# Performance work log

Measured on AMD Instinct MI355X. Metric: run time of the kernel, lower is better.

## Reference

```python
import jax, jax.numpy as jnp
import numpy as np
from jax import lax

BETA = 0.25


def setup_inputs() -> dict:
    key = jax.random.key(0)
    k1, k2 = jax.random.split(key)
    z = jax.random.normal(k1, (16, 64, 32, 32), dtype=jnp.float32)
    # codebook initialized uniform(-1/K, 1/K) in the original; small random is fine for a baseline
    weight = jax.random.uniform(k2, (8192, 64), dtype=jnp.float32, minval=-1.0 / 8192, maxval=1.0 / 8192)
    return {"z": z, "weight": weight}


def reference(z, weight):
    B, D, H, W = z.shape  # D == embedding_dim
    zf = jnp.transpose(z, (0, 2, 3, 1)).reshape(-1, D)  # [N, D]
    # squared L2 distances: ||z||^2 - 2 z.W^T + ||W||^2  -> [N, K]
    dist = (jnp.sum(zf * zf, axis=1, keepdims=True)
            - 2.0 * jnp.matmul(zf, weight.T)
            + jnp.sum(weight * weight, axis=1))
    idx = jnp.argmin(dist, axis=1)  # [N]
    qe = weight[idx]  # [N, D] gather
    quantized = jnp.transpose(qe.reshape(B, H, W, D), (0, 3, 1, 2))  # back to NCHW
    codebook_loss = jnp.mean((qe - lax.stop_gradient(zf)) ** 2)
    commitment_loss = BETA * jnp.mean((zf - lax.stop_gradient(qe)) ** 2)
    # straight-through estimator
    quantized_st = z + lax.stop_gradient(quantized - z)
    return quantized_st, commitment_loss, codebook_loss
```

## Files before the change

### kernel.cpp

```cpp
#include <hip/hip_runtime.h>
#include <hip/hip_bf16.h>
#include <stdint.h>


typedef __bf16 bf16x8 __attribute__((ext_vector_type(8)));
typedef float f32x16 __attribute__((ext_vector_type(16)));

__global__ __launch_bounds__(256)
void vq_prep(const float* __restrict__ w, __bf16* __restrict__ wbf,
             float* __restrict__ wnneg, float* __restrict__ out)
{
  const int i = blockIdx.x * 256 + threadIdx.x;
  const float v = w[i];
  wbf[i] = (__bf16)v;
  float s = v * v;
#pragma unroll
  for (int m = 1; m < 64; m <<= 1) s += __shfl_xor(s, m);
  if ((threadIdx.x & 63) == 0) wnneg[i >> 6] = -0.5f * s;
  if (blockIdx.x == 0 && threadIdx.x < 2) out[1048576 + threadIdx.x] = 0.0f;
}

__global__ __launch_bounds__(512, 2)
void vq_argmax(const float* __restrict__ z, const __bf16* __restrict__ wbf,
               const float* __restrict__ wnneg, float* __restrict__ cand)
{
  __shared__ __align__(16) char bufs[3][16384];
  __shared__ __align__(16) float wnl[1024];
  const int t = threadIdx.x;
  const int lane = t & 63, wv = t >> 6;
  const int hi = lane >> 5, hi4 = hi << 2, rA = lane & 31;
  const int ksp = blockIdx.x & 7, zgrp = blockIdx.x >> 3;
  const int kbase = ksp << 10;
  const int b = zgrp >> 2;
  const int hw0 = (zgrp & 3) << 8;
  const int ch = wv >> 1, rg = wv & 1;

  ((float2*)wnl)[t] = ((const float2*)(wnneg + kbase))[t];
  asm volatile("s_waitcnt lgkmcnt(0)" ::: "memory");

  auto STAGE = [&](int s) {
    char* buf = &bufs[s % 3][0];
    if (s < 4) {
      const char* src = (const char*)z
          + (((size_t)((b << 6) + (s << 4) + wv)) << 12) + (hw0 << 2) + (lane << 4);
      __builtin_amdgcn_global_load_lds(
          (const __attribute__((address_space(1))) void*)src,
          (__attribute__((address_space(3))) void*)(buf + (wv << 10)), 16, 0, 0);
      __builtin_amdgcn_global_load_lds(
          (const __attribute__((address_space(1))) void*)(src + ((size_t)8 << 12)),
          (__attribute__((address_space(3))) void*)(buf + 8192 + (wv << 10)), 16, 0, 0);
    } else {
      const int st = s - 4;
      const int tt = t & 255;
      const int row = tt >> 3, slot = (tt & 7) ^ (row & 7);
      const int q0 = t >> 8, q1 = q0 + 2;
      const char* wb = (const char*)wbf;
      const char* s0 = wb + (((size_t)(kbase + (q0 << 8) + (st << 5) + row)) << 7) + (slot << 4);
      const char* s1 = wb + (((size_t)(kbase + (q1 << 8) + (st << 5) + row)) << 7) + (slot << 4);
      char* d0 = buf + (q0 << 12) + ((wv & 3) << 10);
      char* d1 = buf + (q1 << 12) + ((wv & 3) << 10);
      __builtin_amdgcn_global_load_lds((const __attribute__((address_space(1))) void*)s0,
          (__attribute__((address_space(3))) void*)d0, 16, 0, 0);
      __builtin_amdgcn_global_load_lds((const __attribute__((address_space(1))) void*)s1,
          (__attribute__((address_space(3))) void*)d1, 16, 0, 0);
    }
  };

  STAGE(0); STAGE(1);

  bf16x8 zf[4][4];
#pragma unroll
  for (int c = 0; c < 4; ++c) {
    asm volatile("s_waitcnt vmcnt(2)" ::: "memory");
    asm volatile("s_barrier" ::: "memory");
    const float* zp = (const float*)(&bufs[c % 3][0] + (hi << 13));
#pragma unroll
    for (int nt = 0; nt < 4; ++nt) {
      const int nl = (rg << 7) + (nt << 5) + rA;
      bf16x8 zv;
#pragma unroll
      for (int j = 0; j < 8; ++j) zv[j] = (__bf16)zp[(j << 8) + nl];
      zf[nt][c] = zv;
    }
    STAGE(c + 2);
  }

  float bestpk[4] = {-3.0e38f, -3.0e38f, -3.0e38f, -3.0e38f};

#pragma unroll 1
  for (int i = 4; i < 12; ++i) {
    if (i < 11) asm volatile("s_waitcnt vmcnt(2)" ::: "memory");
    else        asm volatile("s_waitcnt vmcnt(0)" ::: "memory");
    asm volatile("s_barrier" ::: "memory");
    const int st = i - 4;
    const char* tb = &bufs[i % 3][0] + (ch << 12);

    bf16x8 af[4];
#pragma unroll
    for (int ks = 0; ks < 4; ++ks) {
      const int c16 = (ks << 1) + hi;
      af[ks] = *(const bf16x8*)(tb + (rA << 7) + ((c16 ^ (rA & 7)) << 4));
    }

    const int kloc = (ch << 8) + (st << 5);
    f32x16 acc[4];
#pragma unroll
    for (int nt = 0; nt < 4; ++nt) {
      const float4 q0 = *(const float4*)(wnl + kloc + hi4);
      const float4 q1 = *(const float4*)(wnl + kloc + 8 + hi4);
      const float4 q2 = *(const float4*)(wnl + kloc + 16 + hi4);
      const float4 q3 = *(const float4*)(wnl + kloc + 24 + hi4);
      acc[nt] = (f32x16){q0.x, q0.y, q0.z, q0.w, q1.x, q1.y, q1.z, q1.w,
                         q2.x, q2.y, q2.z, q2.w, q3.x, q3.y, q3.z, q3.w};
    }
#pragma unroll
    for (int ks = 0; ks < 4; ++ks) {
#pragma unroll
      for (int nt = 0; nt < 4; ++nt)
        acc[nt] = __builtin_amdgcn_mfma_f32_32x32x16_bf16(af[ks], zf[nt][ks], acc[nt], 0, 0, 0);
    }

    const unsigned khw = (unsigned)(kbase + kloc + hi4);
#pragma unroll
    for (int nt = 0; nt < 4; ++nt) {
      const f32x16 a = acc[nt];
      float pk[16];
#pragma unroll
      for (int r = 0; r < 16; ++r) {
        const unsigned id = khw + (unsigned)((r & 3) + ((r >> 2) << 3));
        pk[r] = __uint_as_float((__float_as_uint(a[r]) & 0xFFFFE000u) | id);
      }
      const float g0 = fmaxf(fmaxf(pk[0], pk[1]), pk[2]);
      const float g1 = fmaxf(fmaxf(pk[3], pk[4]), pk[5]);
      const float g2 = fmaxf(fmaxf(pk[6], pk[7]), pk[8]);
      const float g3 = fmaxf(fmaxf(pk[9], pk[10]), pk[11]);
      const float g4 = fmaxf(fmaxf(pk[12], pk[13]), pk[14]);
      const float h0 = fmaxf(fmaxf(g0, g1), g2);
      const float h1 = fmaxf(fmaxf(g3, g4), pk[15]);
      bestpk[nt] = fmaxf(bestpk[nt], fmaxf(h0, h1));
    }
    if (i < 10) STAGE(i + 2);
  }

  float bp4[4];
#pragma unroll
  for (int nt = 0; nt < 4; ++nt)
    bp4[nt] = fmaxf(bestpk[nt], __shfl_down(bestpk[nt], 32));

  __syncthreads();
  if (lane < 32) {
#pragma unroll
    for (int nt = 0; nt < 4; ++nt)
      wnl[(ch << 8) + (rg << 7) + (nt << 5) + rA] = bp4[nt];
  }
  __syncthreads();
  if (t < 256) {
    const float m = fmaxf(fmaxf(wnl[t], wnl[256 + t]),
                          fmaxf(wnl[512 + t], wnl[768 + t]));
    cand[(ksp << 14) + (zgrp << 8) + t] = m;
  }
}

__global__ __launch_bounds__(256)
void vq_gather(const float* __restrict__ cand, const float* __restrict__ w,
               const float* __restrict__ z, float* __restrict__ out)
{
  const int t = threadIdx.x;
  const int lane = t & 63;
  const int wv = t >> 6;
  const int n = blockIdx.x * 64 + lane;
  float m = cand[n];
#pragma unroll
  for (int k = 1; k < 8; ++k) m = fmaxf(m, cand[(k << 14) + n]);
  const int idx = (int)(__float_as_uint(m) & 8191u);
  const int b = n >> 10, hw = n & 1023;
  const size_t zb = ((size_t)b << 16) | (unsigned)hw;
  const float4* wr = (const float4*)(w + ((size_t)idx << 6));
  float sq = 0.0f;
#pragma unroll
  for (int q = 0; q < 4; ++q) {
    const float4 wvv = wr[(wv << 2) + q];
    const int d0 = (wv << 4) + (q << 2);
#pragma unroll
    for (int j = 0; j < 4; ++j) {
      const float wc = (j == 0) ? wvv.x : (j == 1) ? wvv.y : (j == 2) ? wvv.z : wvv.w;
      const size_t o = zb + ((size_t)(d0 + j) << 10);
      const float df = wc - z[o];
      sq += df * df;
      out[o] = wc;
    }
  }
#pragma unroll
  for (int s2 = 1; s2 < 64; s2 <<= 1) sq += __shfl_xor(sq, s2);
  __shared__ float ps[4];
  if (lane == 0) ps[wv] = sq;
  __syncthreads();
  if (t == 0) {
    const float s = (ps[0] + ps[1] + ps[2] + ps[3]) * (1.0f / 1048576.0f);
    atomicAdd(out + 1048576, 0.25f * s);
    atomicAdd(out + 1048577, s);
  }
}

extern "C" void kernel_launch(void* const* d_in, const int* in_sizes, int n_in,
                              void* d_out, int out_size, void* d_ws, size_t ws_size,
                              hipStream_t stream)
{
  (void)in_sizes; (void)n_in; (void)out_size; (void)ws_size;
  const float* z = (const float*)d_in[0];
  const float* w = (const float*)d_in[1];
  float* out = (float*)d_out;
  char* ws = (char*)d_ws;
  float* cand = (float*)ws;
  __bf16* wbf = (__bf16*)(ws + 524288);
  float* wnneg = (float*)(ws + 524288 + 1048576);

  vq_prep<<<2048, 256, 0, stream>>>(w, wbf, wnneg, out);
  vq_argmax<<<512, 512, 0, stream>>>(z, wbf, wnneg, cand);
  vq_gather<<<256, 256, 0, stream>>>(cand, w, z, out);
}
```

Measured before the change: 44.88 us.

## Pre-transpose z to bf16 fragment layout in prep kernel, deepen codebook pipeline

The prep kernel gains extra blocks that convert z to bf16 and write it in the exact MFMA fragment layout. The argmax kernel can then load its z fragments straight from global memory into registers, instead of staging fp32 z through LDS and converting there. This removes four pipeline stages and their barriers, and frees an LDS buffer so the codebook pipeline becomes four-deep with three tiles in flight. The cost is an extra bf16 write and read of z through the workspace, plus LDS use going from 3 to 4 buffers, which may affect occupancy at 2 blocks per CU.

```diff
diff --git a/kernel.cpp b/kernel.cpp
--- a/kernel.cpp
+++ b/kernel.cpp
@@ -5,96 +5,103 @@
 
 typedef __bf16 bf16x8 __attribute__((ext_vector_type(8)));
 typedef float f32x16 __attribute__((ext_vector_type(16)));
+typedef unsigned int u32x4 __attribute__((ext_vector_type(4)));
 
 __global__ __launch_bounds__(256)
-void vq_prep(const float* __restrict__ w, __bf16* __restrict__ wbf,
-             float* __restrict__ wnneg, float* __restrict__ out)
-{
-  const int i = blockIdx.x * 256 + threadIdx.x;
-  const float v = w[i];
-  wbf[i] = (__bf16)v;
-  float s = v * v;
-#pragma unroll
-  for (int m = 1; m < 64; m <<= 1) s += __shfl_xor(s, m);
-  if ((threadIdx.x & 63) == 0) wnneg[i >> 6] = -0.5f * s;
-  if (blockIdx.x == 0 && threadIdx.x < 2) out[1048576 + threadIdx.x] = 0.0f;
+void vq_prep(const float* __restrict__ w, const float* __restrict__ z,
+             __bf16* __restrict__ wbf, float* __restrict__ wnneg,
+             __bf16* __restrict__ zt, float* __restrict__ out)
+{
+  const int t = threadIdx.x;
+  if (blockIdx.x < 2048) {
+    const int i = blockIdx.x * 256 + t;
+    const float v = w[i];
+    wbf[i] = (__bf16)v;
+    float s = v * v;
+#pragma unroll
+    for (int m = 1; m < 64; m <<= 1) s += __shfl_xor(s, m);
+    if ((t & 63) == 0) wnneg[i >> 6] = -0.5f * s;
+    if (blockIdx.x == 0 && t < 2) out[1048576 + t] = 0.0f;
+  } else {
+    const int bid2 = blockIdx.x - 2048;
+    const int b = bid2 >> 2;
+    const int hw = ((bid2 & 3) << 8) + t;
+    const float* zp = z + (((size_t)b) << 16) + hw;
+    char* ob = (char*)zt + ((((size_t)bid2 << 3) + (t >> 5)) << 12) + ((t & 31) << 4);
+#pragma unroll
+    for (int dc = 0; dc < 8; ++dc) {
+      u32x4 pkt;
+#pragma unroll
+      for (int q = 0; q < 4; ++q) {
+        const float a0 = zp[((size_t)(dc * 8 + q * 2)) << 10];
+        const float a1 = zp[((size_t)(dc * 8 + q * 2 + 1)) << 10];
+        const unsigned short h0 = __builtin_bit_cast(unsigned short, (__bf16)a0);
+        const unsigned short h1 = __builtin_bit_cast(unsigned short, (__bf16)a1);
+        pkt[q] = (unsigned)h0 | ((unsigned)h1 << 16);
+      }
+      *(u32x4*)(ob + (dc << 9)) = pkt;
+    }
+  }
 }
 
 __global__ __launch_bounds__(512, 2)
-void vq_argmax(const float* __restrict__ z, const __bf16* __restrict__ wbf,
+void vq_argmax(const __bf16* __restrict__ zt, const __bf16* __restrict__ wbf,
                const float* __restrict__ wnneg, float* __restrict__ cand)
 {
-  __shared__ __align__(16) char bufs[3][16384];
+  __shared__ __align__(16) char bufs[4][16384];
   __shared__ __align__(16) float wnl[1024];
   const int t = threadIdx.x;
   const int lane = t & 63, wv = t >> 6;
   const int hi = lane >> 5, hi4 = hi << 2, rA = lane & 31;
   const int ksp = blockIdx.x & 7, zgrp = blockIdx.x >> 3;
   const int kbase = ksp << 10;
-  const int b = zgrp >> 2;
-  const int hw0 = (zgrp & 3) << 8;
   const int ch = wv >> 1, rg = wv & 1;
 
   ((float2*)wnl)[t] = ((const float2*)(wnneg + kbase))[t];
   asm volatile("s_waitcnt lgkmcnt(0)" ::: "memory");
 
+  bf16x8 zf[4][4];
+  {
+    const char* zb = (const char*)zt
+        + ((((size_t)(zgrp << 3)) + (rg << 2)) << 12) + (hi << 9) + (rA << 4);
+#pragma unroll
+    for (int nt = 0; nt < 4; ++nt)
+#pragma unroll
+      for (int c = 0; c < 4; ++c)
+        zf[nt][c] = *(const bf16x8*)(zb + (nt << 12) + (c << 10));
+  }
+
+  const int tt = t & 255;
+  const int row = tt >> 3, slot = (tt & 7) ^ (row & 7);
+  const int q0 = t >> 8;
+  const char* s0p = (const char*)wbf
+      + (((size_t)(kbase + (q0 << 8) + row)) << 7) + (slot << 4);
+  const char* s1p = s0p + ((size_t)2 << 15);
+  const int doff0 = (q0 << 12) + ((wv & 3) << 10);
+  const int doff1 = ((q0 + 2) << 12) + ((wv & 3) << 10);
+
   auto STAGE = [&](int s) {
-    char* buf = &bufs[s % 3][0];
-    if (s < 4) {
-      const char* src = (const char*)z
-          + (((size_t)((b << 6) + (s << 4) + wv)) << 12) + (hw0 << 2) + (lane << 4);
-      __builtin_amdgcn_global_load_lds(
-          (const __attribute__((address_space(1))) void*)src,
-          (__attribute__((address_space(3))) void*)(buf + (wv << 10)), 16, 0, 0);
-      __builtin_amdgcn_global_load_lds(
-          (const __attribute__((address_space(1))) void*)(src + ((size_t)8 << 12)),
-          (__attribute__((address_space(3))) void*)(buf + 8192 + (wv << 10)), 16, 0, 0);
-    } else {
-      const int st = s - 4;
-      const int tt = t & 255;
-      const int row = tt >> 3, slot = (tt & 7) ^ (row & 7);
-      const int q0 = t >> 8, q1 = q0 + 2;
-      const char* wb = (const char*)wbf;
-      const char* s0 = wb + (((size_t)(kbase + (q0 << 8) + (st << 5) + row)) << 7) + (slot << 4);
-      const char* s1 = wb + (((size_t)(kbase + (q1 << 8) + (st << 5) + row)) << 7) + (slot << 4);
-      char* d0 = buf + (q0 << 12) + ((wv & 3) << 10);
-      char* d1 = buf + (q1 << 12) + ((wv & 3) << 10);
-      __builtin_amdgcn_global_load_lds((const __attribute__((address_space(1))) void*)s0,
-          (__attribute__((address_space(3))) void*)d0, 16, 0, 0);
-      __builtin_amdgcn_global_load_lds((const __attribute__((address_space(1))) void*)s1,
-          (__attribute__((address_space(3))) void*)d1, 16, 0, 0);
-    }
+    char* buf = &bufs[s & 3][0];
+    __builtin_amdgcn_global_load_lds(
+        (const __attribute__((address_space(1))) void*)(s0p + ((size_t)s << 12)),
+        (__attribute__((address_space(3))) void*)(buf + doff0), 16, 0, 0);
+    __builtin_amdgcn_global_load_lds(
+        (const __attribute__((address_space(1))) void*)(s1p + ((size_t)s << 12)),
+        (__attribute__((address_space(3))) void*)(buf + doff1), 16, 0, 0);
   };
 
-  STAGE(0); STAGE(1);
-
-  bf16x8 zf[4][4];
-#pragma unroll
-  for (int c = 0; c < 4; ++c) {
-    asm volatile("s_waitcnt vmcnt(2)" ::: "memory");
+  STAGE(0); STAGE(1); STAGE(2);
+
+  float bestpk[4] = {-3.0e38f, -3.0e38f, -3.0e38f, -3.0e38f};
+
+#pragma unroll 1
+  for (int i = 0; i < 8; ++i) {
+    if (i < 6)      asm volatile("s_waitcnt vmcnt(4)" ::: "memory");
+    else if (i == 6) asm volatile("s_waitcnt vmcnt(2)" ::: "memory");
+    else            asm volatile("s_waitcnt vmcnt(0)" ::: "memory");
     asm volatile("s_barrier" ::: "memory");
-    const float* zp = (const float*)(&bufs[c % 3][0] + (hi << 13));
-#pragma unroll
-    for (int nt = 0; nt < 4; ++nt) {
-      const int nl = (rg << 7) + (nt << 5) + rA;
-      bf16x8 zv;
-#pragma unroll
-      for (int j = 0; j < 8; ++j) zv[j] = (__bf16)zp[(j << 8) + nl];
-      zf[nt][c] = zv;
-    }
-    STAGE(c + 2);
-  }
-
-  float bestpk[4] = {-3.0e38f, -3.0e38f, -3.0e38f, -3.0e38f};
-
-#pragma unroll 1
-  for (int i = 4; i < 12; ++i) {
-    if (i < 11) asm volatile("s_waitcnt vmcnt(2)" ::: "memory");
-    else        asm volatile("s_waitcnt vmcnt(0)" ::: "memory");
-    asm volatile("s_barrier" ::: "memory");
-    const int st = i - 4;
-    const char* tb = &bufs[i % 3][0] + (ch << 12);
-
+
+    const char* tb = &bufs[i & 3][0] + (ch << 12);
     bf16x8 af[4];
 #pragma unroll
     for (int ks = 0; ks < 4; ++ks) {
@@ -102,16 +109,16 @@
       af[ks] = *(const bf16x8*)(tb + (rA << 7) + ((c16 ^ (rA & 7)) << 4));
     }
 
-    const int kloc = (ch << 8) + (st << 5);
+    const int kloc = (ch << 8) + (i << 5);
     f32x16 acc[4];
 #pragma unroll
     for (int nt = 0; nt < 4; ++nt) {
-      const float4 q0 = *(const float4*)(wnl + kloc + hi4);
-      const float4 q1 = *(const float4*)(wnl + kloc + 8 + hi4);
-      const float4 q2 = *(const float4*)(wnl + kloc + 16 + hi4);
-      const float4 q3 = *(const float4*)(wnl + kloc + 24 + hi4);
-      acc[nt] = (f32x16){q0.x, q0.y, q0.z, q0.w, q1.x, q1.y, q1.z, q1.w,
-                         q2.x, q2.y, q2.z, q2.w, q3.x, q3.y, q3.z, q3.w};
+      const float4 b0 = *(const float4*)(wnl + kloc + hi4);
+      const float4 b1 = *(const float4*)(wnl + kloc + 8 + hi4);
+      const float4 b2 = *(const float4*)(wnl + kloc + 16 + hi4);
+      const float4 b3 = *(const float4*)(wnl + kloc + 24 + hi4);
+      acc[nt] = (f32x16){b0.x, b0.y, b0.z, b0.w, b1.x, b1.y, b1.z, b1.w,
+                         b2.x, b2.y, b2.z, b2.w, b3.x, b3.y, b3.z, b3.w};
     }
 #pragma unroll
     for (int ks = 0; ks < 4; ++ks) {
@@ -139,7 +146,7 @@
       const float h1 = fmaxf(fmaxf(g3, g4), pk[15]);
       bestpk[nt] = fmaxf(bestpk[nt], fmaxf(h0, h1));
     }
-    if (i < 10) STAGE(i + 2);
+    if (i < 5) STAGE(i + 3);
   }
 
   float bp4[4];
@@ -214,8 +221,9 @@
   float* cand = (float*)ws;
   __bf16* wbf = (__bf16*)(ws + 524288);
   float* wnneg = (float*)(ws + 524288 + 1048576);
-
-  vq_prep<<<2048, 256, 0, stream>>>(w, wbf, wnneg, out);
-  vq_argmax<<<512, 512, 0, stream>>>(z, wbf, wnneg, cand);
+  __bf16* zt = (__bf16*)(ws + 524288 + 1048576 + 32768);
+
+  vq_prep<<<2112, 256, 0, stream>>>(w, z, wbf, wnneg, zt, out);
+  vq_argmax<<<512, 512, 0, stream>>>(zt, wbf, wnneg, cand);
   vq_gather<<<256, 256, 0, stream>>>(cand, w, z, out);
 }
```

Result: no change. 44.16 us (-1.6%).
